# Kernel optimization log

Measured on AMD Instinct MI355X. Metric: run time of the kernel, lower is better.

The kernel has to match this reference:

```python
import jax, jax.numpy as jnp
import numpy as np

N = 50000      # nodes (batched molecular graphs)
E = 800000     # edges
G = 2048       # graphs in the batch
IN = 128       # in_channels
H = 128        # hidden
EPS = 1e-5     # BatchNorm eps


def _glorot(key, shape):
    lim = float(np.sqrt(6.0 / (shape[0] + shape[1])))
    return jax.random.uniform(key, shape, jnp.float32, -lim, lim)


def setup_inputs() -> dict:
    key = jax.random.key(0)
    ks = jax.random.split(key, 8)
    x = jax.random.normal(ks[0], (N, IN), jnp.float32)
    edge_index = jax.random.randint(ks[1], (2, E), 0, N, dtype=jnp.int64)
    batch = jnp.sort(jax.random.randint(ks[2], (N,), 0, G, dtype=jnp.int64))
    return {
        "x": x,
        "edge_index": edge_index,
        "batch": batch,
        "W1": _glorot(ks[3], (IN, H)), "b1": jnp.zeros((H,), jnp.float32),
        "gamma1": jnp.ones((H,), jnp.float32), "beta1": jnp.zeros((H,), jnp.float32),
        "W2": _glorot(ks[4], (H, H)), "b2": jnp.zeros((H,), jnp.float32),
        "gamma2": jnp.ones((H,), jnp.float32), "beta2": jnp.zeros((H,), jnp.float32),
        "Wout": _glorot(ks[5], (H, 1)), "bout": jnp.zeros((1,), jnp.float32),
    }


def gcn_conv(x, src, dst, W, b):
    # PyG GCNConv: add self-loops, symmetric norm D^-1/2 (A+I) D^-1/2, transform-first.
    n = x.shape[0]
    loop = jnp.arange(n, dtype=src.dtype)
    s = jnp.concatenate([src, loop])           # [E+N]
    d = jnp.concatenate([dst, loop])
    deg = jax.ops.segment_sum(jnp.ones_like(d, jnp.float32), d, num_segments=n)
    dinv = jnp.where(deg > 0, jax.lax.rsqrt(deg), 0.0)
    norm = dinv[s] * dinv[d]                   # [E+N]
    xw = x @ W                                 # [N, H] transform first (cheaper)
    msg = xw[s] * norm[:, None]                # [E+N, H] gathered, normalized messages
    out = jax.ops.segment_sum(msg, d, num_segments=n)  # scatter-add aggregate
    return out + b


def batch_norm(x, gamma, beta):
    # BatchNorm1d training-mode forward: batch stats, biased variance.
    mean = jnp.mean(x, axis=0)
    var = jnp.mean(jnp.square(x - mean), axis=0)
    return (x - mean) * jax.lax.rsqrt(var + EPS) * gamma + beta


def reference(x, edge_index, batch, W1, b1, gamma1, beta1, W2, b2, gamma2, beta2, Wout, bout):
    src, dst = edge_index[0], edge_index[1]
    h = jax.nn.relu(batch_norm(gcn_conv(x, src, dst, W1, b1), gamma1, beta1))
    h = jax.nn.relu(batch_norm(gcn_conv(h, src, dst, W2, b2), gamma2, beta2))
    # global_mean_pool over graph ids
    sums = jax.ops.segment_sum(h, batch, num_segments=G)            # [G, H]
    cnts = jax.ops.segment_sum(jnp.ones((h.shape[0],), h.dtype), batch, num_segments=G)
    pooled = sums / jnp.maximum(cnts, 1.0)[:, None]
    return pooled @ Wout + bout                                     # [G, 1]
```

## Files before the change

### kernel.cpp

```cpp
#include <hip/hip_runtime.h>
#include <stdint.h>

#define HD 128
#define EPS 1e-5f
#define NPB 256
#define SENT 0xFFFFFFFFu

typedef __attribute__((ext_vector_type(8))) short bf16x8;
typedef __attribute__((ext_vector_type(4))) float f32x4;

__device__ inline unsigned bf_round(float f) {
  unsigned u = __float_as_uint(f);
  return (u + 0x7fffu + ((u >> 16) & 1u)) >> 16;
}
__device__ inline unsigned bf_pack2(float x, float y) {
  return bf_round(x) | (bf_round(y) << 16);
}
__device__ inline float2 bf_unpack2(unsigned u) {
  float2 r;
  r.x = __uint_as_float(u << 16);
  r.y = __uint_as_float(u & 0xffff0000u);
  return r;
}
__device__ inline float bf_up(unsigned short us) {
  return __uint_as_float(((unsigned)us) << 16);
}

__global__ void k_prep(const float* __restrict__ W1, const float* __restrict__ W2,
                       unsigned short* __restrict__ Wt1, unsigned short* __restrict__ Wt2,
                       int* __restrict__ bline, float* __restrict__ sums1,
                       float* __restrict__ sums2, int nbline) {
  int b = blockIdx.x, t = threadIdx.x;
  if (b < 64) {
    int e = b * 256 + t;
    int k = e >> 7, c = e & 127;
    Wt1[c * 128 + k] = (unsigned short)bf_round(W1[e]);
  } else if (b < 128) {
    int e = (b - 64) * 256 + t;
    int k = e >> 7, c = e & 127;
    Wt2[c * 128 + k] = (unsigned short)bf_round(W2[e]);
  } else {
    int i = (b - 128) * 256 + t;
    if (i < nbline) bline[i] = 0;
    if (i < 256) { sums1[i] = 0.f; sums2[i] = 0.f; }
  }
}

__global__ __launch_bounds__(256) void k_phaseA(const int* __restrict__ src, const int* __restrict__ dst,
                                                int* __restrict__ bline, unsigned* __restrict__ arena,
                                                int E, int NBKT, int capLines, int chunk) {
  __shared__ int hist[NPB], gbase[NPB], ccap[NPB], lpos[NPB];
  const int t = threadIdx.x;
  for (int i = t; i < NPB; i += 256) { hist[i] = 0; lpos[i] = 0; }
  __syncthreads();
  const int e0 = blockIdx.x * chunk;
  const int e1 = (e0 + chunk < E) ? e0 + chunk : E;
  for (int i = e0 + t; i < e1; i += 256) atomicAdd(&hist[dst[i] >> 8], 1);
  __syncthreads();
  for (int b = t; b < NBKT; b += 256) {
    int n = hist[b];
    int nl = (n + 15) >> 4;
    int base = nl ? atomicAdd(&bline[b * 16], nl) : 0;
    if (base + nl > capLines) nl = (base < capLines) ? capLines - base : 0;
    gbase[b] = b * capLines * 16 + base * 16;
    ccap[b] = nl * 16;
  }
  __syncthreads();
  for (int i = e0 + t; i < e1; i += 256) {
    int d = dst[i];
    int b = d >> 8;
    int lp = atomicAdd(&lpos[b], 1);
    if (lp < ccap[b]) arena[gbase[b] + lp] = ((unsigned)src[i] << 8) | (unsigned)(d & 255);
  }
  __syncthreads();
  for (int b = t; b < NBKT; b += 256) {
    int n = lpos[b] < ccap[b] ? lpos[b] : ccap[b];
    for (int j = n; j < ccap[b]; ++j) arena[gbase[b] + j] = SENT;
  }
}

__global__ __launch_bounds__(256) void k_phaseB(const unsigned* __restrict__ arena,
                                                const int* __restrict__ bline,
                                                unsigned short* __restrict__ colidx,
                                                unsigned* __restrict__ nodeinfo,
                                                float* __restrict__ dinv,
                                                int N, int capLines) {
  __shared__ int deg[NPB], pos[NPB], scan[NPB];
  const int b = blockIdx.x;
  const int t = threadIdx.x;
  deg[t] = 0;
  __syncthreads();
  int used = bline[b * 16];
  if (used > capLines) used = capLines;
  const int slots = used * 16;
  const unsigned* seg = arena + (size_t)b * capLines * 16;
  for (int s = t; s < slots; s += 256) {
    unsigned u = seg[s];
    if (u != SENT) atomicAdd(&deg[u & 255], 1);
  }
  __syncthreads();
  int v = deg[t];
  scan[t] = v;
  __syncthreads();
  for (int off = 1; off < 256; off <<= 1) {
    int tv = (t >= off) ? scan[t - off] : 0;
    __syncthreads();
    scan[t] += tv;
    __syncthreads();
  }
  int prefix = scan[t] - v;
  pos[t] = prefix;
  int n = b * NPB + t;
  if (n < N) {
    unsigned off = (unsigned)(b * capLines * 16 + prefix);
    unsigned d8 = (unsigned)(v < 255 ? v : 255);
    nodeinfo[n] = (off << 8) | d8;
    dinv[n] = rsqrtf((float)v + 1.0f);
  }
  __syncthreads();
  unsigned short* cseg = colidx + (size_t)b * capLines * 16;
  for (int s = t; s < slots; s += 256) {
    unsigned u = seg[s];
    if (u != SENT) {
      int p = atomicAdd(&pos[u & 255], 1);
      cseg[p] = (unsigned short)(u >> 8);
    }
  }
}

#define SAB_LD 136
__global__ __launch_bounds__(256) void k_gemm(const float* __restrict__ Af32,
                                              const unsigned short* __restrict__ Abf,
                                              const unsigned short* __restrict__ Wt,
                                              unsigned short* __restrict__ Yp, int N,
                                              const float* __restrict__ dinv,
                                              const float* __restrict__ sums,
                                              const float* __restrict__ gamma,
                                              const float* __restrict__ beta, float invN) {
  __shared__ unsigned short sWt[128 * SAB_LD];
  __shared__ float sSc[128], sSh[128];
  const int tid = threadIdx.x;
  const int row0 = blockIdx.x * 64;
  for (int i = tid * 8; i < 128 * 128; i += 256 * 8) {
    int c = i >> 7, k = i & 127;
    *(uint4*)&sWt[c * SAB_LD + k] = *(const uint4*)&Wt[i];
  }
  if (sums && tid < 128) {
    float mean = sums[tid] * invN;
    float var = sums[128 + tid] * invN - mean * mean;
    float sc = gamma[tid] * rsqrtf(var + EPS);
    sSc[tid] = sc;
    sSh[tid] = beta[tid] - mean * sc;
  }
  __syncthreads();
  const int w = tid >> 6;
  const int l = tid & 63;
  const int lr = l & 15;
  const int lk = (l >> 4) * 8;
  const int arow = row0 + w * 16 + lr;
  const bool rv = arow < N;
  f32x4 acc[8];
#pragma unroll
  for (int t = 0; t < 8; ++t) acc[t] = (f32x4){0.f, 0.f, 0.f, 0.f};
#pragma unroll
  for (int kk = 0; kk < 128; kk += 32) {
    bf16x8 af;
    if (!Abf) {
      float4 f0 = make_float4(0.f, 0.f, 0.f, 0.f), f1 = f0;
      if (rv) {
        f0 = *(const float4*)&Af32[(size_t)arow * HD + kk + lk];
        f1 = *(const float4*)&Af32[(size_t)arow * HD + kk + lk + 4];
      }
      af[0] = (short)bf_round(f0.x); af[1] = (short)bf_round(f0.y);
      af[2] = (short)bf_round(f0.z); af[3] = (short)bf_round(f0.w);
      af[4] = (short)bf_round(f1.x); af[5] = (short)bf_round(f1.y);
      af[6] = (short)bf_round(f1.z); af[7] = (short)bf_round(f1.w);
    } else {
      bf16x8 raw = (bf16x8){0, 0, 0, 0, 0, 0, 0, 0};
      if (rv) raw = *(const bf16x8*)&Abf[(size_t)arow * HD + kk + lk];
      float4 c0 = *(const float4*)&sSc[kk + lk];
      float4 c1 = *(const float4*)&sSc[kk + lk + 4];
      float4 h0 = *(const float4*)&sSh[kk + lk];
      float4 h1 = *(const float4*)&sSh[kk + lk + 4];
      float vv;
#define BNAPP(i, sc, sh) \
      vv = bf_up((unsigned short)raw[i]); \
      vv = fmaxf(0.f, vv * (sc) + (sh)); \
      af[i] = (short)bf_round(vv);
      BNAPP(0, c0.x, h0.x) BNAPP(1, c0.y, h0.y) BNAPP(2, c0.z, h0.z) BNAPP(3, c0.w, h0.w)
      BNAPP(4, c1.x, h1.x) BNAPP(5, c1.y, h1.y) BNAPP(6, c1.z, h1.z) BNAPP(7, c1.w, h1.w)
#undef BNAPP
    }
#pragma unroll
    for (int t = 0; t < 8; ++t) {
      bf16x8 bfr = *(const bf16x8*)&sWt[(t * 16 + lr) * SAB_LD + kk + lk];
      acc[t] = __builtin_amdgcn_mfma_f32_16x16x32_bf16(af, bfr, acc[t], 0, 0, 0);
    }
  }
  const int rbase = row0 + w * 16 + (l >> 4) * 4;
#pragma unroll
  for (int j = 0; j < 4; ++j) {
    int r = rbase + j;
    if (r >= N) continue;
    float d = dinv[r];
#pragma unroll
    for (int t = 0; t < 8; ++t) {
      Yp[(size_t)r * HD + t * 16 + lr] = (unsigned short)bf_round(acc[t][j] * d);
    }
  }
}

__global__ __launch_bounds__(256) void k_aggregate(const unsigned* __restrict__ Yp,
                                                   const unsigned* __restrict__ nodeinfo,
                                                   const unsigned short* __restrict__ colidx,
                                                   const float* __restrict__ dinv,
                                                   unsigned* __restrict__ Out, int N) {
  int n = (blockIdx.x * blockDim.x + threadIdx.x) >> 6;
  int lane = threadIdx.x & 63;
  if (n >= N) return;
  const int sl = lane & 31;
  const int hid = lane >> 5;
  const unsigned info = nodeinfo[n];
  const int beg = (int)(info >> 8);
  const int deg = (int)(info & 255);
  float a0 = 0.f, a1 = 0.f, a2 = 0.f, a3 = 0.f;
  if (hid == 0) {
    uint2 u = *(const uint2*)&Yp[(size_t)n * 64 + sl * 2];
    float2 p0 = bf_unpack2(u.x), p1 = bf_unpack2(u.y);
    a0 = p0.x; a1 = p0.y; a2 = p1.x; a3 = p1.y;
  }
  for (int base = 0; base < deg; base += 64) {
    int cnt = deg - base; if (cnt > 64) cnt = 64;
    int nbr = (lane < cnt) ? (int)colidx[beg + base + lane] : 0;
    int j = 0;
    for (; j + 16 <= cnt; j += 16) {
      int s0 = __shfl(nbr, j + 0 + hid, 64);
      int s1 = __shfl(nbr, j + 2 + hid, 64);
      int s2 = __shfl(nbr, j + 4 + hid, 64);
      int s3 = __shfl(nbr, j + 6 + hid, 64);
      int s4 = __shfl(nbr, j + 8 + hid, 64);
      int s5 = __shfl(nbr, j + 10 + hid, 64);
      int s6 = __shfl(nbr, j + 12 + hid, 64);
      int s7 = __shfl(nbr, j + 14 + hid, 64);
      uint2 q0 = *(const uint2*)&Yp[(size_t)s0 * 64 + sl * 2];
      uint2 q1 = *(const uint2*)&Yp[(size_t)s1 * 64 + sl * 2];
      uint2 q2 = *(const uint2*)&Yp[(size_t)s2 * 64 + sl * 2];
      uint2 q3 = *(const uint2*)&Yp[(size_t)s3 * 64 + sl * 2];
      uint2 q4 = *(const uint2*)&Yp[(size_t)s4 * 64 + sl * 2];
      uint2 q5 = *(const uint2*)&Yp[(size_t)s5 * 64 + sl * 2];
      uint2 q6 = *(const uint2*)&Yp[(size_t)s6 * 64 + sl * 2];
      uint2 q7 = *(const uint2*)&Yp[(size_t)s7 * 64 + sl * 2];
      float2 x0 = bf_unpack2(q0.x), y0 = bf_unpack2(q0.y);
      float2 x1 = bf_unpack2(q1.x), y1 = bf_unpack2(q1.y);
      float2 x2 = bf_unpack2(q2.x), y2 = bf_unpack2(q2.y);
      float2 x3 = bf_unpack2(q3.x), y3 = bf_unpack2(q3.y);
      float2 x4 = bf_unpack2(q4.x), y4 = bf_unpack2(q4.y);
      float2 x5 = bf_unpack2(q5.x), y5 = bf_unpack2(q5.y);
      float2 x6 = bf_unpack2(q6.x), y6 = bf_unpack2(q6.y);
      float2 x7 = bf_unpack2(q7.x), y7 = bf_unpack2(q7.y);
      a0 += ((x0.x + x1.x) + (x2.x + x3.x)) + ((x4.x + x5.x) + (x6.x + x7.x));
      a1 += ((x0.y + x1.y) + (x2.y + x3.y)) + ((x4.y + x5.y) + (x6.y + x7.y));
      a2 += ((y0.x + y1.x) + (y2.x + y3.x)) + ((y4.x + y5.x) + (y6.x + y7.x));
      a3 += ((y0.y + y1.y) + (y2.y + y3.y)) + ((y4.y + y5.y) + (y6.y + y7.y));
    }
    for (; j + 2 <= cnt; j += 2) {
      int s = __shfl(nbr, j + hid, 64);
      uint2 q = *(const uint2*)&Yp[(size_t)s * 64 + sl * 2];
      float2 x = bf_unpack2(q.x), y = bf_unpack2(q.y);
      a0 += x.x; a1 += x.y; a2 += y.x; a3 += y.y;
    }
    if (j < cnt) {
      int s = __shfl(nbr, j, 64);
      if (hid == 0) {
        uint2 q = *(const uint2*)&Yp[(size_t)s * 64 + sl * 2];
        float2 x = bf_unpack2(q.x), y = bf_unpack2(q.y);
        a0 += x.x; a1 += x.y; a2 += y.x; a3 += y.y;
      }
    }
  }
  a0 += __shfl_xor(a0, 32, 64);
  a1 += __shfl_xor(a1, 32, 64);
  a2 += __shfl_xor(a2, 32, 64);
  a3 += __shfl_xor(a3, 32, 64);
  if (hid == 0) {
    float dd = dinv[n];
    unsigned lo = bf_pack2(a0 * dd, a1 * dd);
    unsigned hi = bf_pack2(a2 * dd, a3 * dd);
    *(uint2*)&Out[(size_t)n * 64 + sl * 2] = make_uint2(lo, hi);
  }
}

__global__ __launch_bounds__(256) void k_colstats(const unsigned* __restrict__ X, int N,
                                                  float* __restrict__ sums) {
  const int c2 = threadIdx.x & 63;
  const int half = threadIdx.x >> 6;
  float sx = 0.f, sy = 0.f, qx = 0.f, qy = 0.f;
  for (int r = blockIdx.x * 4 + half; r < N; r += gridDim.x * 4) {
    float2 v = bf_unpack2(X[(size_t)r * 64 + c2]);
    sx += v.x; sy += v.y; qx += v.x * v.x; qy += v.y * v.y;
  }
  __shared__ float l0[256], l1[256], l2[256], l3[256];
  l0[threadIdx.x] = sx; l1[threadIdx.x] = sy; l2[threadIdx.x] = qx; l3[threadIdx.x] = qy;
  __syncthreads();
  if (threadIdx.x < 64) {
    int t = threadIdx.x;
    sx = l0[t] + l0[t + 64] + l0[t + 128] + l0[t + 192];
    sy = l1[t] + l1[t + 64] + l1[t + 128] + l1[t + 192];
    qx = l2[t] + l2[t + 64] + l2[t + 128] + l2[t + 192];
    qy = l3[t] + l3[t + 64] + l3[t + 128] + l3[t + 192];
    int c = t * 2;
    atomicAdd(&sums[c], sx);
    atomicAdd(&sums[c + 1], sy);
    atomicAdd(&sums[128 + c], qx);
    atomicAdd(&sums[129 + c], qy);
  }
}

__global__ __launch_bounds__(256) void k_finalnode(const unsigned* __restrict__ Agg,
                                                   const float* __restrict__ sums,
                                                   const float* __restrict__ gamma,
                                                   const float* __restrict__ beta,
                                                   const float* __restrict__ wout,
                                                   float* __restrict__ nodescalar,
                                                   int N, float invN) {
  int n = (blockIdx.x * blockDim.x + threadIdx.x) >> 6;
  int lane = threadIdx.x & 63;
  if (n >= N) return;
  int c = lane * 2;
  float mean0 = sums[c] * invN;
  float var0 = sums[128 + c] * invN - mean0 * mean0;
  float sc0 = gamma[c] * rsqrtf(var0 + EPS);
  float sh0 = beta[c] - mean0 * sc0;
  float mean1 = sums[c + 1] * invN;
  float var1 = sums[129 + c] * invN - mean1 * mean1;
  float sc1 = gamma[c + 1] * rsqrtf(var1 + EPS);
  float sh1 = beta[c + 1] - mean1 * sc1;
  float2 v = bf_unpack2(Agg[(size_t)n * 64 + lane]);
  float h0 = fmaxf(0.f, v.x * sc0 + sh0);
  float h1 = fmaxf(0.f, v.y * sc1 + sh1);
  float p = h0 * wout[c] + h1 * wout[c + 1];
  for (int off = 32; off > 0; off >>= 1) p += __shfl_down(p, off);
  if (lane == 0) nodescalar[n] = p;
}

__global__ void k_finalout(const float* __restrict__ nodescalar, const int* __restrict__ batch,
                           const float* __restrict__ bout, float* __restrict__ out,
                           int G, int N) {
  int g = blockIdx.x * blockDim.x + threadIdx.x;
  if (g >= G) return;
  int lo = 0, hi = N;
  while (lo < hi) { int mid = (lo + hi) >> 1; if (batch[mid] < g) lo = mid + 1; else hi = mid; }
  int lb = lo;
  hi = N;
  while (lo < hi) { int mid = (lo + hi) >> 1; if (batch[mid] <= g) lo = mid + 1; else hi = mid; }
  float s = 0.f;
  for (int i = lb; i < lo; ++i) s += nodescalar[i];
  float cnt = (float)(lo - lb);
  out[g] = s / fmaxf(cnt, 1.0f) + bout[0];
}

extern "C" void kernel_launch(void* const* d_in, const int* in_sizes, int n_in,
                              void* d_out, int out_size, void* d_ws, size_t ws_size,
                              hipStream_t stream) {
  (void)n_in; (void)ws_size;
  const float* x      = (const float*)d_in[0];
  const int*   ei     = (const int*)d_in[1];
  const int*   batch  = (const int*)d_in[2];
  const float* W1     = (const float*)d_in[3];
  const float* gamma1 = (const float*)d_in[5];
  const float* beta1  = (const float*)d_in[6];
  const float* W2     = (const float*)d_in[7];
  const float* gamma2 = (const float*)d_in[9];
  const float* beta2  = (const float*)d_in[10];
  const float* wout   = (const float*)d_in[11];
  const float* bout   = (const float*)d_in[12];
  float* out = (float*)d_out;

  const int N = in_sizes[0] / HD;
  const int E = in_sizes[1] / 2;
  const int G = out_size;
  const int* src = ei;
  const int* dst = ei + E;
  const int NBKT = (N + NPB - 1) / NPB;
  const int NWGA = 256;
  const int chunk = (E + NWGA - 1) / NWGA;
  const int capLines = E / (NBKT * 16) + NWGA + 64;
  const int capSlots = capLines * 16;
  const float invN = 1.0f / (float)N;

  char* p = (char*)d_ws;
  auto carve = [&](size_t bytes) { char* r = p; p += (bytes + 255) & ~(size_t)255; return r; };
  unsigned* bufY = (unsigned*)carve((size_t)N * 64 * 4);
  unsigned* bufAgg = (unsigned*)carve((size_t)N * 64 * 4);
  unsigned* arena = (unsigned*)carve((size_t)NBKT * capSlots * 4);
  unsigned short* colidx = (unsigned short*)carve((size_t)NBKT * capSlots * 2);
  unsigned short* Wt1 = (unsigned short*)carve(128 * 128 * 2);
  unsigned short* Wt2 = (unsigned short*)carve(128 * 128 * 2);
  unsigned* nodeinfo = (unsigned*)carve((size_t)N * 4);
  float* dinv    = (float*)carve((size_t)N * 4);
  float* nodescalar = (float*)carve((size_t)N * 4);
  int*   bline = (int*)carve((size_t)NBKT * 16 * 4);
  float* sums1 = (float*)carve(256 * 4);
  float* sums2 = (float*)carve(256 * 4);

  const int nbline = NBKT * 16;
  const int pblocks = 128 + (nbline + 255) / 256;
  k_prep<<<pblocks, 256, 0, stream>>>(W1, W2, Wt1, Wt2, bline, sums1, sums2, nbline);

  k_phaseA<<<NWGA, 256, 0, stream>>>(src, dst, bline, arena, E, NBKT, capLines, chunk);
  k_phaseB<<<NBKT, 256, 0, stream>>>(arena, bline, colidx, nodeinfo, dinv, N, capLines);

  const int gblocks = (N + 63) / 64;
  const int ablocks = (N + 3) / 4;
  k_gemm<<<gblocks, 256, 0, stream>>>(x, nullptr, Wt1, (unsigned short*)bufY, N, dinv,
                                      nullptr, nullptr, nullptr, invN);
  k_aggregate<<<ablocks, 256, 0, stream>>>(bufY, nodeinfo, colidx, dinv, bufAgg, N);
  k_colstats<<<512, 256, 0, stream>>>(bufAgg, N, sums1);
  k_gemm<<<gblocks, 256, 0, stream>>>(nullptr, (const unsigned short*)bufAgg, Wt2,
                                      (unsigned short*)bufY, N, dinv, sums1, gamma1, beta1, invN);
  k_aggregate<<<ablocks, 256, 0, stream>>>(bufY, nodeinfo, colidx, dinv, bufAgg, N);
  k_colstats<<<512, 256, 0, stream>>>(bufAgg, N, sums2);
  k_finalnode<<<ablocks, 256, 0, stream>>>(bufAgg, sums2, gamma2, beta2, wout, nodescalar, N, invN);
  k_finalout<<<(G + 255) / 256, 256, 0, stream>>>(nodescalar, batch, bout, out, G, N);
}
```

Baseline: 216.8 us.

## Cache edges in registers, enlarge GEMM tiles, fuse mean-pool into final node kernel

```diff
diff --git a/kernel.cpp b/kernel.cpp
--- a/kernel.cpp
+++ b/kernel.cpp
@@ -5,6 +5,7 @@
 #define EPS 1e-5f
 #define NPB 256
 #define SENT 0xFFFFFFFFu
+#define MAXE 16
 
 typedef __attribute__((ext_vector_type(8))) short bf16x8;
 typedef __attribute__((ext_vector_type(4))) float f32x4;
@@ -29,7 +30,10 @@
 __global__ void k_prep(const float* __restrict__ W1, const float* __restrict__ W2,
                        unsigned short* __restrict__ Wt1, unsigned short* __restrict__ Wt2,
                        int* __restrict__ bline, float* __restrict__ sums1,
-                       float* __restrict__ sums2, int nbline) {
+                       float* __restrict__ sums2, int nbline,
+                       const int* __restrict__ batch, float* __restrict__ invcnt,
+                       const float* __restrict__ bout, float* __restrict__ out,
+                       int G, int N, int zblocks) {
   int b = blockIdx.x, t = threadIdx.x;
   if (b < 64) {
     int e = b * 256 + t;
@@ -39,10 +43,22 @@
     int e = (b - 64) * 256 + t;
     int k = e >> 7, c = e & 127;
     Wt2[c * 128 + k] = (unsigned short)bf_round(W2[e]);
-  } else {
+  } else if (b < 128 + zblocks) {
     int i = (b - 128) * 256 + t;
     if (i < nbline) bline[i] = 0;
     if (i < 256) { sums1[i] = 0.f; sums2[i] = 0.f; }
+  } else {
+    int g = (b - 128 - zblocks) * 256 + t;
+    if (g < G) {
+      int lo = 0, hi = N;
+      while (lo < hi) { int mid = (lo + hi) >> 1; if (batch[mid] < g) lo = mid + 1; else hi = mid; }
+      int lb = lo;
+      hi = N;
+      while (lo < hi) { int mid = (lo + hi) >> 1; if (batch[mid] <= g) lo = mid + 1; else hi = mid; }
+      float cnt = (float)(lo - lb);
+      invcnt[g] = 1.0f / fmaxf(cnt, 1.0f);
+      out[g] = bout[0];
+    }
   }
 }
 
@@ -55,7 +71,19 @@
   __syncthreads();
   const int e0 = blockIdx.x * chunk;
   const int e1 = (e0 + chunk < E) ? e0 + chunk : E;
-  for (int i = e0 + t; i < e1; i += 256) atomicAdd(&hist[dst[i] >> 8], 1);
+  unsigned ec[MAXE];
+#pragma unroll
+  for (int it = 0; it < MAXE; ++it) {
+    int i = e0 + it * 256 + t;
+    ec[it] = SENT;
+    if (i < e1) {
+      int d = dst[i];
+      int s = src[i];
+      int bk = d >> 8;
+      ec[it] = ((unsigned)bk << 24) | ((unsigned)s << 8) | (unsigned)(d & 255);
+      atomicAdd(&hist[bk], 1);
+    }
+  }
   __syncthreads();
   for (int b = t; b < NBKT; b += 256) {
     int n = hist[b];
@@ -66,11 +94,14 @@
     ccap[b] = nl * 16;
   }
   __syncthreads();
-  for (int i = e0 + t; i < e1; i += 256) {
-    int d = dst[i];
-    int b = d >> 8;
-    int lp = atomicAdd(&lpos[b], 1);
-    if (lp < ccap[b]) arena[gbase[b] + lp] = ((unsigned)src[i] << 8) | (unsigned)(d & 255);
+#pragma unroll
+  for (int it = 0; it < MAXE; ++it) {
+    unsigned u = ec[it];
+    if (u != SENT) {
+      int b = (int)(u >> 24);
+      int lp = atomicAdd(&lpos[b], 1);
+      if (lp < ccap[b]) arena[gbase[b] + lp] = u & 0x00FFFFFFu;
+    }
   }
   __syncthreads();
   for (int b = t; b < NBKT; b += 256) {
@@ -129,7 +160,7 @@
 }
 
 #define SAB_LD 136
-__global__ __launch_bounds__(256) void k_gemm(const float* __restrict__ Af32,
+__global__ __launch_bounds__(512) void k_gemm(const float* __restrict__ Af32,
                                               const unsigned short* __restrict__ Abf,
                                               const unsigned short* __restrict__ Wt,
                                               unsigned short* __restrict__ Yp, int N,
@@ -140,8 +171,8 @@
   __shared__ unsigned short sWt[128 * SAB_LD];
   __shared__ float sSc[128], sSh[128];
   const int tid = threadIdx.x;
-  const int row0 = blockIdx.x * 64;
-  for (int i = tid * 8; i < 128 * 128; i += 256 * 8) {
+  const int row0 = blockIdx.x * 128;
+  for (int i = tid * 8; i < 128 * 128; i += 512 * 8) {
     int c = i >> 7, k = i & 127;
     *(uint4*)&sWt[c * SAB_LD + k] = *(const uint4*)&Wt[i];
   }
@@ -321,7 +352,9 @@
                                                    const float* __restrict__ gamma,
                                                    const float* __restrict__ beta,
                                                    const float* __restrict__ wout,
-                                                   float* __restrict__ nodescalar,
+                                                   const int* __restrict__ batch,
+                                                   const float* __restrict__ invcnt,
+                                                   float* __restrict__ out,
                                                    int N, float invN) {
   int n = (blockIdx.x * blockDim.x + threadIdx.x) >> 6;
   int lane = threadIdx.x & 63;
@@ -340,23 +373,10 @@
   float h1 = fmaxf(0.f, v.y * sc1 + sh1);
   float p = h0 * wout[c] + h1 * wout[c + 1];
   for (int off = 32; off > 0; off >>= 1) p += __shfl_down(p, off);
-  if (lane == 0) nodescalar[n] = p;
-}
-
-__global__ void k_finalout(const float* __restrict__ nodescalar, const int* __restrict__ batch,
-                           const float* __restrict__ bout, float* __restrict__ out,
-                           int G, int N) {
-  int g = blockIdx.x * blockDim.x + threadIdx.x;
-  if (g >= G) return;
-  int lo = 0, hi = N;
-  while (lo < hi) { int mid = (lo + hi) >> 1; if (batch[mid] < g) lo = mid + 1; else hi = mid; }
-  int lb = lo;
-  hi = N;
-  while (lo < hi) { int mid = (lo + hi) >> 1; if (batch[mid] <= g) lo = mid + 1; else hi = mid; }
-  float s = 0.f;
-  for (int i = lb; i < lo; ++i) s += nodescalar[i];
-  float cnt = (float)(lo - lb);
-  out[g] = s / fmaxf(cnt, 1.0f) + bout[0];
+  if (lane == 0) {
+    int g = batch[n];
+    atomicAdd(&out[g], p * invcnt[g]);
+  }
 }
 
 extern "C" void kernel_launch(void* const* d_in, const int* in_sizes, int n_in,
@@ -398,28 +418,31 @@
   unsigned short* Wt2 = (unsigned short*)carve(128 * 128 * 2);
   unsigned* nodeinfo = (unsigned*)carve((size_t)N * 4);
   float* dinv    = (float*)carve((size_t)N * 4);
-  float* nodescalar = (float*)carve((size_t)N * 4);
+  float* invcnt  = (float*)carve((size_t)G * 4);
   int*   bline = (int*)carve((size_t)NBKT * 16 * 4);
   float* sums1 = (float*)carve(256 * 4);
   float* sums2 = (float*)carve(256 * 4);
 
   const int nbline = NBKT * 16;
-  const int pblocks = 128 + (nbline + 255) / 256;
-  k_prep<<<pblocks, 256, 0, stream>>>(W1, W2, Wt1, Wt2, bline, sums1, sums2, nbline);
+  const int zblocks = (nbline + 255) / 256;
+  const int gb2 = (G + 255) / 256;
+  const int pblocks = 128 + zblocks + gb2;
+  k_prep<<<pblocks, 256, 0, stream>>>(W1, W2, Wt1, Wt2, bline, sums1, sums2, nbline,
+                                      batch, invcnt, bout, out, G, N, zblocks);
 
   k_phaseA<<<NWGA, 256, 0, stream>>>(src, dst, bline, arena, E, NBKT, capLines, chunk);
   k_phaseB<<<NBKT, 256, 0, stream>>>(arena, bline, colidx, nodeinfo, dinv, N, capLines);
 
-  const int gblocks = (N + 63) / 64;
+  const int gblocks = (N + 127) / 128;
   const int ablocks = (N + 3) / 4;
-  k_gemm<<<gblocks, 256, 0, stream>>>(x, nullptr, Wt1, (unsigned short*)bufY, N, dinv,
+  k_gemm<<<gblocks, 512, 0, stream>>>(x, nullptr, Wt1, (unsigned short*)bufY, N, dinv,
                                       nullptr, nullptr, nullptr, invN);
   k_aggregate<<<ablocks, 256, 0, stream>>>(bufY, nodeinfo, colidx, dinv, bufAgg, N);
   k_colstats<<<512, 256, 0, stream>>>(bufAgg, N, sums1);
-  k_gemm<<<gblocks, 256, 0, stream>>>(nullptr, (const unsigned short*)bufAgg, Wt2,
+  k_gemm<<<gblocks, 512, 0, stream>>>(nullptr, (const unsigned short*)bufAgg, Wt2,
                                       (unsigned short*)bufY, N, dinv, sums1, gamma1, beta1, invN);
   k_aggregate<<<ablocks, 256, 0, stream>>>(bufY, nodeinfo, colidx, dinv, bufAgg, N);
   k_colstats<<<512, 256, 0, stream>>>(bufAgg, N, sums2);
-  k_finalnode<<<ablocks, 256, 0, stream>>>(bufAgg, sums2, gamma2, beta2, wout, nodescalar, N, invN);
-  k_finalout<<<(G + 255) / 256, 256, 0, stream>>>(nodescalar, batch, bout, out, G, N);
-}
+  k_finalnode<<<ablocks, 256, 0, stream>>>(bufAgg, sums2, gamma2, beta2, wout, batch,
+                                           invcnt, out, N, invN);
+}
```

New measurement: 224.9 us. 1.04x slower.
